# Performance work log

Hardware: AMD Instinct MI355X
Metric: run time of the kernel (lower is better)

The kernel has to match this reference:

```python
import jax, jax.numpy as jnp
import numpy as np
from jax import lax

B, D_IN, LOW_DIM, NUM_CLASS, MOCO_QUEUE = 4096, 1024, 128, 32, 65536
PROTO_M, MOCO_M, EPS = 0.99, 0.999, 1e-12


def l2norm(x, axis=-1):
    n = jnp.linalg.norm(x, axis=axis, keepdims=True)
    return x / jnp.maximum(n, EPS)


def encoder(x, W_cls, b_cls, W_proj):
    # base_encoder returns (class logits, l2-normalized low-dim embedding)
    return x @ W_cls + b_cls, l2norm(x @ W_proj)


def setup_inputs() -> dict:
    key = jax.random.key(0)
    k = jax.random.split(key, 12)
    img_q = jax.random.normal(k[0], (B, D_IN), jnp.float32)
    im_k = jax.random.normal(k[1], (B, D_IN), jnp.float32)
    true_lab = jax.random.randint(k[2], (B,), 0, NUM_CLASS)
    partial_Y = (jax.random.uniform(k[3], (B, NUM_CLASS)) < 0.3).astype(jnp.float32)
    partial_Y = partial_Y.at[jnp.arange(B), true_lab].set(1.0)  # guarantee nonempty candidate set
    W_cls_q = 0.02 * jax.random.normal(k[4], (D_IN, NUM_CLASS), jnp.float32)
    b_cls_q = jnp.zeros((NUM_CLASS,), jnp.float32)
    W_proj_q = 0.02 * jax.random.normal(k[5], (D_IN, LOW_DIM), jnp.float32)
    # key encoder initialized near query encoder (copied then momentum-drifted)
    W_cls_k = W_cls_q + 0.002 * jax.random.normal(k[6], (D_IN, NUM_CLASS), jnp.float32)
    b_cls_k = jnp.zeros((NUM_CLASS,), jnp.float32)
    W_proj_k = W_proj_q + 0.002 * jax.random.normal(k[7], (D_IN, LOW_DIM), jnp.float32)
    queue = jax.random.normal(k[8], (MOCO_QUEUE, LOW_DIM), jnp.float32)
    queue = queue / jnp.maximum(jnp.linalg.norm(queue, axis=0, keepdims=True), EPS)  # F.normalize(queue, dim=0) as in __init__
    queue_pseudo = jax.random.normal(k[9], (MOCO_QUEUE, NUM_CLASS), jnp.float32)
    queue_partial = jax.random.normal(k[10], (MOCO_QUEUE, NUM_CLASS), jnp.float32)
    prototypes = l2norm(jax.random.normal(k[11], (NUM_CLASS, LOW_DIM), jnp.float32))
    return dict(img_q=img_q, im_k=im_k, partial_Y=partial_Y,
                W_cls_q=W_cls_q, b_cls_q=b_cls_q, W_proj_q=W_proj_q,
                W_cls_k=W_cls_k, b_cls_k=b_cls_k, W_proj_k=W_proj_k,
                prototypes=prototypes, queue=queue,
                queue_pseudo=queue_pseudo, queue_partial=queue_partial)


def reference(img_q, im_k, partial_Y, W_cls_q, b_cls_q, W_proj_q,
              W_cls_k, b_cls_k, W_proj_k, prototypes, queue,
              queue_pseudo, queue_partial):
    output, q = encoder(img_q, W_cls_q, b_cls_q, W_proj_q)
    predicted_scores = jax.nn.softmax(output, axis=1) * partial_Y
    pseudo_labels = jnp.argmax(predicted_scores, axis=1)  # (B,) int
    # prototypes are detached before the similarity (clone().detach())
    score_prot = jax.nn.softmax(q @ lax.stop_gradient(prototypes).T, axis=1)
    # order-dependent per-sample EMA scatter (faithful to the python for-loop,
    # including within-batch label collisions) -> lax.scan recurrence
    qd = lax.stop_gradient(q)
    def step(p, xs):
        feat, lab = xs
        return p.at[lab].set(p[lab] * PROTO_M + (1.0 - PROTO_M) * feat), None
    new_protos, _ = lax.scan(step, lax.stop_gradient(prototypes), (qd, pseudo_labels))
    new_protos = l2norm(new_protos)
    # momentum key-encoder update (no grad), then key features
    Wck = lax.stop_gradient(W_cls_k * MOCO_M + W_cls_q * (1.0 - MOCO_M))
    bck = lax.stop_gradient(b_cls_k * MOCO_M + b_cls_q * (1.0 - MOCO_M))
    Wpk = lax.stop_gradient(W_proj_k * MOCO_M + W_proj_q * (1.0 - MOCO_M))
    _, kfeat = encoder(im_k, Wck, bck, Wpk)
    kfeat = lax.stop_gradient(kfeat)
    qv = lax.stop_gradient(queue)
    qp = lax.stop_gradient(queue_pseudo)
    qpt = lax.stop_gradient(queue_partial)
    features = jnp.concatenate([q, kfeat, qv], axis=0)
    pseudo_scores = jnp.concatenate([predicted_scores, predicted_scores, qp], axis=0)
    partial_target = jnp.concatenate([partial_Y, partial_Y, qpt], axis=0)
    # dequeue-and-enqueue at ptr=0 (buffer state update, no grad)
    new_queue = qv.at[0:B].set(kfeat)
    new_queue_pseudo = qp.at[0:B].set(lax.stop_gradient(predicted_scores))
    new_queue_partial = qpt.at[0:B].set(lax.stop_gradient(partial_Y))
    return (output, features, pseudo_scores, partial_target, score_prot,
            new_protos, new_queue, new_queue_pseudo, new_queue_partial)
```

## Files before the change

kernel.cpp:

```cpp
#include <hip/hip_runtime.h>
#include <hip/hip_bf16.h>
#include <stdint.h>


typedef __attribute__((ext_vector_type(8))) short bf16x8;
typedef __attribute__((ext_vector_type(4))) float f32x4;

constexpr size_t O0 = 0;
constexpr size_t O1 = 131072;
constexpr size_t O2 = 9568256;
constexpr size_t O3 = 11927552;
constexpr size_t O4 = 14286848;
constexpr size_t O5 = 14417920;
constexpr size_t O6 = 14422016;
constexpr size_t O7 = 22810624;
constexpr size_t O8 = 24907776;

__device__ __forceinline__ unsigned short f2b(float x) {
  union { float f; uint32_t u; } v; v.f = x;
  uint32_t u = v.u;
  uint32_t r = (u + 0x7fffu + ((u >> 16) & 1u)) >> 16;
  return (unsigned short)r;
}

__global__ __launch_bounds__(256) void prep_w(const float* __restrict__ W1,
                                              const float* __restrict__ W2,
                                              float a1, float a2, int N,
                                              unsigned short* __restrict__ Wt) {
  __shared__ float tile[32][33];
  const int kb = blockIdx.x * 32, nb = blockIdx.y * 32;
  const int tx = threadIdx.x, ty = threadIdx.y;
#pragma unroll
  for (int j = 0; j < 4; ++j) {
    const int k = kb + ty + 8 * j;
    float v = W1[(size_t)k * N + nb + tx] * a1;
    if (W2) v += W2[(size_t)k * N + nb + tx] * a2;
    tile[ty + 8 * j][tx] = v;
  }
  __syncthreads();
#pragma unroll
  for (int j = 0; j < 4; ++j) {
    const int n = nb + ty + 8 * j;
    Wt[(size_t)n * 1024 + kb + tx] = f2b(tile[tx][ty + 8 * j]);
  }
}

template <int NWAVES>
__global__ __launch_bounds__(NWAVES * 64) void gemm_enc(
    const float* __restrict__ A, const unsigned short* __restrict__ Wt,
    float* __restrict__ C) {
  constexpr int BN = NWAVES * 32;
  constexpr int NT = NWAVES * 64;
  constexpr int K = 1024;
  __shared__ __align__(16) unsigned char sA[16 * 128];
  __shared__ __align__(16) unsigned char sB[BN * 128];
  const int t = threadIdx.x;
  const int w = t >> 6, l = t & 63;
  const int ar = l & 15, kg = l >> 4;
  const int cs = w * 32;
  const int m0 = blockIdx.x * 16;
  f32x4 acc0 = {0.f, 0.f, 0.f, 0.f}, acc1 = {0.f, 0.f, 0.f, 0.f};
  for (int k0 = 0; k0 < K; k0 += 64) {
    if (t < 256) {
      const int r = t >> 4;
      const int c8 = (t & 15) * 8;
      const float4 v = *(const float4*)(A + (size_t)(m0 + r) * K + k0 + (t & 15) * 4);
      uint2 pk;
      pk.x = (uint32_t)f2b(v.x) | ((uint32_t)f2b(v.y) << 16);
      pk.y = (uint32_t)f2b(v.z) | ((uint32_t)f2b(v.w) << 16);
      *(uint2*)(sA + ((r * 128 + c8) ^ ((r & 7) << 4))) = pk;
    }
#pragma unroll
    for (int i = 0; i < (BN * 8) / NT; ++i) {
      const int cid = t + i * NT;
      const int r = cid >> 3, c = cid & 7;
      const uint4 v = *(const uint4*)(Wt + (size_t)r * K + k0 + c * 8);
      *(uint4*)(sB + ((r * 128 + c * 16) ^ ((r & 7) << 4))) = v;
    }
    __syncthreads();
#pragma unroll
    for (int s = 0; s < 2; ++s) {
      const int ch = (s * 4 + kg) * 16;
      bf16x8 a = *(const bf16x8*)(sA + ((ar * 128 + ch) ^ ((ar & 7) << 4)));
      const int r0 = cs + ar, r1 = cs + 16 + ar;
      bf16x8 b0 = *(const bf16x8*)(sB + ((r0 * 128 + ch) ^ ((r0 & 7) << 4)));
      bf16x8 b1 = *(const bf16x8*)(sB + ((r1 * 128 + ch) ^ ((r1 & 7) << 4)));
      acc0 = __builtin_amdgcn_mfma_f32_16x16x32_bf16(a, b0, acc0, 0, 0, 0);
      acc1 = __builtin_amdgcn_mfma_f32_16x16x32_bf16(a, b1, acc1, 0, 0, 0);
    }
    __syncthreads();
  }
#pragma unroll
  for (int j = 0; j < 4; ++j) {
    const int row = m0 + kg * 4 + j;
    C[(size_t)row * BN + cs + ar] = acc0[j];
    C[(size_t)row * BN + cs + 16 + ar] = acc1[j];
  }
}

__global__ __launch_bounds__(256) void post_q(
    const float* __restrict__ CQ, const float* __restrict__ bias,
    const float* __restrict__ partialY, const float* __restrict__ protos,
    float* __restrict__ out, int* __restrict__ labels) {
  __shared__ float pr[32 * 129];
  __shared__ float qs[4][128];
  const int t = threadIdx.x;
  for (int i = t; i < 4096; i += 256) pr[(i >> 7) * 129 + (i & 127)] = protos[i];
  __syncthreads();
  const int w = t >> 6, l = t & 63;
  const int row = blockIdx.x * 4 + w;
  const float* cq = CQ + (size_t)row * 160;

  float logit = -1e30f;
  if (l < 32) logit = cq[128 + l] + bias[l];
  float m = logit;
  for (int o = 32; o; o >>= 1) m = fmaxf(m, __shfl_xor(m, o));
  const float e = (l < 32) ? __expf(logit - m) : 0.f;
  float ssum = e;
  for (int o = 32; o; o >>= 1) ssum += __shfl_xor(ssum, o);
  const float py = (l < 32) ? partialY[(size_t)row * 32 + l] : 0.f;
  const float p = e / ssum * py;
  if (l < 32) {
    out[O0 + (size_t)row * 32 + l] = logit;
    out[O2 + (size_t)row * 32 + l] = p;
    out[O2 + (size_t)(4096 + row) * 32 + l] = p;
    out[O7 + (size_t)row * 32 + l] = p;
    out[O3 + (size_t)row * 32 + l] = py;
    out[O3 + (size_t)(4096 + row) * 32 + l] = py;
    out[O8 + (size_t)row * 32 + l] = py;
  }
  float av = (l < 32) ? p : -1.f;
  int ai = (l < 32) ? l : 1000;
  for (int o = 32; o; o >>= 1) {
    const float ov = __shfl_xor(av, o);
    const int oi = __shfl_xor(ai, o);
    if (ov > av || (ov == av && oi < ai)) { av = ov; ai = oi; }
  }
  if (l == 0) labels[row] = ai;

  float v0 = cq[l], v1 = cq[64 + l];
  float ss = v0 * v0 + v1 * v1;
  for (int o = 32; o; o >>= 1) ss += __shfl_xor(ss, o);
  const float den = fmaxf(sqrtf(ss), 1e-12f);
  v0 /= den; v1 /= den;
  out[O1 + (size_t)row * 128 + l] = v0;
  out[O1 + (size_t)row * 128 + 64 + l] = v1;
  qs[w][l] = v0;
  qs[w][64 + l] = v1;

  const int c = l & 31;
  const int dh = (l >> 5) * 64;
  float acc = 0.f;
#pragma unroll
  for (int d = 0; d < 64; ++d) acc += qs[w][dh + d] * pr[c * 129 + dh + d];
  acc += __shfl_xor(acc, 32);
  float sm = acc;
  for (int o = 16; o; o >>= 1) sm = fmaxf(sm, __shfl_xor(sm, o));
  const float ee = __expf(acc - sm);
  float s2 = ee;
  for (int o = 16; o; o >>= 1) s2 += __shfl_xor(s2, o);
  if (l < 32) out[O4 + (size_t)row * 32 + l] = ee / s2;
}

__global__ __launch_bounds__(256) void post_k(const float* __restrict__ CK,
                                              float* __restrict__ out) {
  const int t = threadIdx.x, w = t >> 6, l = t & 63;
  const int row = blockIdx.x * 4 + w;
  const float* ck = CK + (size_t)row * 128;
  float v0 = ck[l], v1 = ck[64 + l];
  float ss = v0 * v0 + v1 * v1;
  for (int o = 32; o; o >>= 1) ss += __shfl_xor(ss, o);
  const float den = fmaxf(sqrtf(ss), 1e-12f);
  v0 /= den; v1 /= den;
  out[O1 + (size_t)(4096 + row) * 128 + l] = v0;
  out[O1 + (size_t)(4096 + row) * 128 + 64 + l] = v1;
  out[O6 + (size_t)row * 128 + l] = v0;
  out[O6 + (size_t)row * 128 + 64 + l] = v1;
}

__global__ __launch_bounds__(128) void proto_up(const int* __restrict__ labels,
                                                const float* __restrict__ qfeat,
                                                const float* __restrict__ protos,
                                                float* __restrict__ out) {
  __shared__ int lab[4096];
  __shared__ int list[4096];
  __shared__ int cnt[128];
  __shared__ int ktot;
  __shared__ float red[2];
  const int c = blockIdx.x, t = threadIdx.x;
  for (int i = t; i < 4096; i += 128) lab[i] = labels[i];
  __syncthreads();
  int cn = 0;
#pragma unroll
  for (int j = 0; j < 32; ++j) {
    const int jj = (j + t) & 31;
    cn += (lab[t * 32 + jj] == c) ? 1 : 0;
  }
  cnt[t] = cn;
  __syncthreads();
  if (t == 0) {
    int s = 0;
    for (int i = 0; i < 128; ++i) { const int v = cnt[i]; cnt[i] = s; s += v; }
    ktot = s;
  }
  __syncthreads();
  int off = cnt[t];
  for (int j = 0; j < 32; ++j) {
    const int i = t * 32 + j;
    if (lab[i] == c) list[off++] = i;
  }
  __syncthreads();
  const int k = ktot;
  float* wf = (float*)lab;
  for (int j = t; j < k; j += 128)
    wf[j] = 0.01f * __powf(0.99f, (float)(k - 1 - j));
  __syncthreads();
  float acc = protos[(size_t)c * 128 + t] * __powf(0.99f, (float)k);
  for (int j = 0; j < k; ++j)
    acc += wf[j] * qfeat[(size_t)list[j] * 128 + t];
  float ss = acc * acc;
  for (int o = 32; o; o >>= 1) ss += __shfl_xor(ss, o);
  if ((t & 63) == 0) red[t >> 6] = ss;
  __syncthreads();
  const float tot = red[0] + red[1];
  out[O5 + (size_t)c * 128 + t] = acc / fmaxf(sqrtf(tot), 1e-12f);
}

__global__ __launch_bounds__(256) void copy_bufs(const float* __restrict__ queue,
                                                 const float* __restrict__ qp,
                                                 const float* __restrict__ qpt,
                                                 float* __restrict__ out) {
  constexpr long NQ4 = (long)65536 * 128 / 4;
  constexpr long NP4 = (long)65536 * 32 / 4;
  constexpr long TOT = NQ4 + 2 * NP4;
  float4* o4 = (float4*)out;
  for (long idx = (long)blockIdx.x * blockDim.x + threadIdx.x; idx < TOT;
       idx += (long)gridDim.x * blockDim.x) {
    if (idx < NQ4) {
      const float4 v = ((const float4*)queue)[idx];
      o4[O1 / 4 + (2L * 4096 * 128) / 4 + idx] = v;
      if ((idx >> 5) >= 4096) o4[O6 / 4 + idx] = v;
    } else if (idx < NQ4 + NP4) {
      const long i = idx - NQ4;
      const float4 v = ((const float4*)qp)[i];
      o4[O2 / 4 + (2L * 4096 * 32) / 4 + i] = v;
      if ((i >> 3) >= 4096) o4[O7 / 4 + i] = v;
    } else {
      const long i = idx - NQ4 - NP4;
      const float4 v = ((const float4*)qpt)[i];
      o4[O3 / 4 + (2L * 4096 * 32) / 4 + i] = v;
      if ((i >> 3) >= 4096) o4[O8 / 4 + i] = v;
    }
  }
}

extern "C" void kernel_launch(void* const* d_in, const int* in_sizes, int n_in,
                              void* d_out, int out_size, void* d_ws, size_t ws_size,
                              hipStream_t stream) {
  const float* img_q    = (const float*)d_in[0];
  const float* im_k     = (const float*)d_in[1];
  const float* partialY = (const float*)d_in[2];
  const float* W_cls_q  = (const float*)d_in[3];
  const float* b_cls_q  = (const float*)d_in[4];
  const float* W_proj_q = (const float*)d_in[5];
  const float* W_proj_k = (const float*)d_in[8];
  const float* protos   = (const float*)d_in[9];
  const float* queue    = (const float*)d_in[10];
  const float* queue_ps = (const float*)d_in[11];
  const float* queue_pt = (const float*)d_in[12];
  float* out = (float*)d_out;

  unsigned short* wtq = (unsigned short*)d_ws;
  unsigned short* wtk = wtq + 160 * 1024;
  float* CQ = (float*)(wtk + 128 * 1024);
  float* CK = CQ + (size_t)4096 * 160;
  int* labels = (int*)(CK + (size_t)4096 * 128);

  prep_w<<<dim3(32, 4), dim3(32, 8), 0, stream>>>(W_proj_q, nullptr, 1.0f, 0.0f, 128, wtq);
  prep_w<<<dim3(32, 1), dim3(32, 8), 0, stream>>>(W_cls_q, nullptr, 1.0f, 0.0f, 32, wtq + 128 * 1024);
  prep_w<<<dim3(32, 4), dim3(32, 8), 0, stream>>>(W_proj_k, W_proj_q, 0.999f, 0.001f, 128, wtk);
  gemm_enc<5><<<256, 320, 0, stream>>>(img_q, wtq, CQ);
  gemm_enc<4><<<256, 256, 0, stream>>>(im_k, wtk, CK);
  post_q<<<1024, 256, 0, stream>>>(CQ, b_cls_q, partialY, protos, out, labels);
  post_k<<<1024, 256, 0, stream>>>(CK, out);
  proto_up<<<32, 128, 0, stream>>>(labels, out + O1, protos, out);
  copy_bufs<<<2048, 256, 0, stream>>>(queue, queue_ps, queue_pt, out);
}
```

Baseline: 262.6 us.

## Fuse launches into prep/gemm/post kernels with split-K atomics and register prefetch

Folds the three weight-prep launches into one kernel that also zeroes the accumulation buffers, and merges both encoder GEMMs plus the classifier GEMM into a single launch. The GEMMs use split-K over two halves with atomic adds, and prefetch the next k-tile into registers while the current one is computed. The q/k postprocessing and the queue copy are merged into one launch. proto_up uses a wave-scan prefix sum and a four-way unrolled accumulation. This cuts launch count and raises GEMM parallelism, at the cost of extra zeroing traffic, atomic contention and nondeterministic summation order.

```diff
diff --git a/kernel.cpp b/kernel.cpp
--- a/kernel.cpp
+++ b/kernel.cpp
@@ -23,13 +23,34 @@
   return (unsigned short)r;
 }
 
-__global__ __launch_bounds__(256) void prep_w(const float* __restrict__ W1,
-                                              const float* __restrict__ W2,
-                                              float a1, float a2, int N,
-                                              unsigned short* __restrict__ Wt) {
+__global__ __launch_bounds__(256) void prep_zero(
+    const float* __restrict__ Wpq, const float* __restrict__ Wcq,
+    const float* __restrict__ Wpk,
+    unsigned short* __restrict__ wt_pq, unsigned short* __restrict__ wt_cls,
+    unsigned short* __restrict__ wt_pk, float* __restrict__ zbase) {
+  const int bid = blockIdx.x;
+  const int t = threadIdx.x;
+  if (bid >= 288) {
+    constexpr int ZN4 = 4096 * (128 + 32 + 128) / 4;
+    float4* z = (float4*)zbase;
+    const float4 zero = {0.f, 0.f, 0.f, 0.f};
+    for (int i = (bid - 288) * 256 + t; i < ZN4; i += 256 * 256) z[i] = zero;
+    return;
+  }
+  const float *W1, *W2 = nullptr;
+  float a1 = 1.f, a2 = 0.f;
+  unsigned short* dst;
+  int kb, nb, N;
+  if (bid < 128) {
+    W1 = Wpq; N = 128; kb = (bid & 31) * 32; nb = (bid >> 5) * 32; dst = wt_pq;
+  } else if (bid < 160) {
+    W1 = Wcq; N = 32; kb = (bid - 128) * 32; nb = 0; dst = wt_cls;
+  } else {
+    W1 = Wpk; W2 = Wpq; a1 = 0.999f; a2 = 0.001f; N = 128;
+    const int b = bid - 160; kb = (b & 31) * 32; nb = (b >> 5) * 32; dst = wt_pk;
+  }
   __shared__ float tile[32][33];
-  const int kb = blockIdx.x * 32, nb = blockIdx.y * 32;
-  const int tx = threadIdx.x, ty = threadIdx.y;
+  const int tx = t & 31, ty = t >> 5;
 #pragma unroll
   for (int j = 0; j < 4; ++j) {
     const int k = kb + ty + 8 * j;
@@ -41,141 +62,240 @@
 #pragma unroll
   for (int j = 0; j < 4; ++j) {
     const int n = nb + ty + 8 * j;
-    Wt[(size_t)n * 1024 + kb + tx] = f2b(tile[tx][ty + 8 * j]);
-  }
-}
-
-template <int NWAVES>
-__global__ __launch_bounds__(NWAVES * 64) void gemm_enc(
-    const float* __restrict__ A, const unsigned short* __restrict__ Wt,
-    float* __restrict__ C) {
-  constexpr int BN = NWAVES * 32;
-  constexpr int NT = NWAVES * 64;
-  constexpr int K = 1024;
-  __shared__ __align__(16) unsigned char sA[16 * 128];
-  __shared__ __align__(16) unsigned char sB[BN * 128];
+    dst[(size_t)n * 1024 + kb + tx] = f2b(tile[tx][ty + 8 * j]);
+  }
+}
+
+__global__ __launch_bounds__(256) void gemm_all(
+    const float* __restrict__ img_q, const float* __restrict__ im_k,
+    const unsigned short* __restrict__ wt_pq,
+    const unsigned short* __restrict__ wt_pk,
+    const unsigned short* __restrict__ wt_cls,
+    float* __restrict__ CQ, float* __restrict__ CK, float* __restrict__ CL) {
+  __shared__ __align__(16) unsigned char lds[18432];
+  const int bid = blockIdx.x;
   const int t = threadIdx.x;
   const int w = t >> 6, l = t & 63;
   const int ar = l & 15, kg = l >> 4;
-  const int cs = w * 32;
-  const int m0 = blockIdx.x * 16;
-  f32x4 acc0 = {0.f, 0.f, 0.f, 0.f}, acc1 = {0.f, 0.f, 0.f, 0.f};
-  for (int k0 = 0; k0 < K; k0 += 64) {
-    if (t < 256) {
-      const int r = t >> 4;
-      const int c8 = (t & 15) * 8;
-      const float4 v = *(const float4*)(A + (size_t)(m0 + r) * K + k0 + (t & 15) * 4);
-      uint2 pk;
-      pk.x = (uint32_t)f2b(v.x) | ((uint32_t)f2b(v.y) << 16);
-      pk.y = (uint32_t)f2b(v.z) | ((uint32_t)f2b(v.w) << 16);
-      *(uint2*)(sA + ((r * 128 + c8) ^ ((r & 7) << 4))) = pk;
-    }
-#pragma unroll
-    for (int i = 0; i < (BN * 8) / NT; ++i) {
-      const int cid = t + i * NT;
-      const int r = cid >> 3, c = cid & 7;
-      const uint4 v = *(const uint4*)(Wt + (size_t)r * K + k0 + c * 8);
-      *(uint4*)(sB + ((r * 128 + c * 16) ^ ((r & 7) << 4))) = v;
-    }
-    __syncthreads();
-#pragma unroll
-    for (int s = 0; s < 2; ++s) {
-      const int ch = (s * 4 + kg) * 16;
-      bf16x8 a = *(const bf16x8*)(sA + ((ar * 128 + ch) ^ ((ar & 7) << 4)));
-      const int r0 = cs + ar, r1 = cs + 16 + ar;
-      bf16x8 b0 = *(const bf16x8*)(sB + ((r0 * 128 + ch) ^ ((r0 & 7) << 4)));
-      bf16x8 b1 = *(const bf16x8*)(sB + ((r1 * 128 + ch) ^ ((r1 & 7) << 4)));
-      acc0 = __builtin_amdgcn_mfma_f32_16x16x32_bf16(a, b0, acc0, 0, 0, 0);
-      acc1 = __builtin_amdgcn_mfma_f32_16x16x32_bf16(a, b1, acc1, 0, 0, 0);
-    }
-    __syncthreads();
-  }
-#pragma unroll
-  for (int j = 0; j < 4; ++j) {
-    const int row = m0 + kg * 4 + j;
-    C[(size_t)row * BN + cs + ar] = acc0[j];
-    C[(size_t)row * BN + cs + 16 + ar] = acc1[j];
-  }
-}
-
-__global__ __launch_bounds__(256) void post_q(
-    const float* __restrict__ CQ, const float* __restrict__ bias,
+
+  if (bid < 1024) {
+    const bool isq = bid < 512;
+    const int b = bid & 511;
+    const int m0 = (b & 255) * 16;
+    const int kb = (b >> 8) * 512;
+    const float* A = isq ? img_q : im_k;
+    const unsigned short* Wt = isq ? wt_pq : wt_pk;
+    float* C = isq ? CQ : CK;
+    unsigned char* sA = lds;
+    unsigned char* sB = lds + 2048;
+    const int arow = t >> 4, acol = t & 15;
+    f32x4 acc0 = {0.f, 0.f, 0.f, 0.f}, acc1 = {0.f, 0.f, 0.f, 0.f};
+    float4 av; uint4 bv[4];
+    av = *(const float4*)(A + (size_t)(m0 + arow) * 1024 + kb + acol * 4);
+#pragma unroll
+    for (int i = 0; i < 4; ++i) {
+      const int cid = t + i * 256, r = cid >> 3, c = cid & 7;
+      bv[i] = *(const uint4*)(Wt + (size_t)r * 1024 + kb + c * 8);
+    }
+    for (int it = 0; it < 8; ++it) {
+      {
+        uint2 pk;
+        pk.x = (uint32_t)f2b(av.x) | ((uint32_t)f2b(av.y) << 16);
+        pk.y = (uint32_t)f2b(av.z) | ((uint32_t)f2b(av.w) << 16);
+        *(uint2*)(sA + ((arow * 128 + acol * 8) ^ ((arow & 7) << 4))) = pk;
+      }
+#pragma unroll
+      for (int i = 0; i < 4; ++i) {
+        const int cid = t + i * 256, r = cid >> 3, c = cid & 7;
+        *(uint4*)(sB + ((r * 128 + c * 16) ^ ((r & 7) << 4))) = bv[i];
+      }
+      if (it < 7) {
+        const int k0 = kb + (it + 1) * 64;
+        av = *(const float4*)(A + (size_t)(m0 + arow) * 1024 + k0 + acol * 4);
+#pragma unroll
+        for (int i = 0; i < 4; ++i) {
+          const int cid = t + i * 256, r = cid >> 3, c = cid & 7;
+          bv[i] = *(const uint4*)(Wt + (size_t)r * 1024 + k0 + c * 8);
+        }
+      }
+      __syncthreads();
+      const int cs = w * 32;
+#pragma unroll
+      for (int s = 0; s < 2; ++s) {
+        const int ch = (s * 4 + kg) * 16;
+        bf16x8 a = *(const bf16x8*)(sA + ((ar * 128 + ch) ^ ((ar & 7) << 4)));
+        const int r0 = cs + ar, r1 = cs + 16 + ar;
+        bf16x8 b0 = *(const bf16x8*)(sB + ((r0 * 128 + ch) ^ ((r0 & 7) << 4)));
+        bf16x8 b1 = *(const bf16x8*)(sB + ((r1 * 128 + ch) ^ ((r1 & 7) << 4)));
+        acc0 = __builtin_amdgcn_mfma_f32_16x16x32_bf16(a, b0, acc0, 0, 0, 0);
+        acc1 = __builtin_amdgcn_mfma_f32_16x16x32_bf16(a, b1, acc1, 0, 0, 0);
+      }
+      __syncthreads();
+    }
+    const int cs = w * 32;
+#pragma unroll
+    for (int j = 0; j < 4; ++j) {
+      const int row = m0 + kg * 4 + j;
+      unsafeAtomicAdd(&C[(size_t)row * 128 + cs + ar], acc0[j]);
+      unsafeAtomicAdd(&C[(size_t)row * 128 + cs + 16 + ar], acc1[j]);
+    }
+  } else {
+    const int b2 = bid - 1024;
+    const int m0 = (b2 & 63) * 64;
+    const int kb = (b2 >> 6) * 512;
+    unsigned char* sA = lds;
+    unsigned char* sB = lds + 8192;
+    f32x4 acc0 = {0.f, 0.f, 0.f, 0.f}, acc1 = {0.f, 0.f, 0.f, 0.f};
+    float4 av[4]; uint4 bv;
+#pragma unroll
+    for (int i = 0; i < 4; ++i) {
+      const int cid = t + i * 256, r = cid >> 4, c = cid & 15;
+      av[i] = *(const float4*)(img_q + (size_t)(m0 + r) * 1024 + kb + c * 4);
+    }
+    { const int r = t >> 3, c = t & 7;
+      bv = *(const uint4*)(wt_cls + (size_t)r * 1024 + kb + c * 8); }
+    for (int it = 0; it < 8; ++it) {
+#pragma unroll
+      for (int i = 0; i < 4; ++i) {
+        const int cid = t + i * 256, r = cid >> 4, c8 = (cid & 15) * 8;
+        uint2 pk;
+        pk.x = (uint32_t)f2b(av[i].x) | ((uint32_t)f2b(av[i].y) << 16);
+        pk.y = (uint32_t)f2b(av[i].z) | ((uint32_t)f2b(av[i].w) << 16);
+        *(uint2*)(sA + ((r * 128 + c8) ^ ((r & 7) << 4))) = pk;
+      }
+      { const int r = t >> 3, c = t & 7;
+        *(uint4*)(sB + ((r * 128 + c * 16) ^ ((r & 7) << 4))) = bv; }
+      if (it < 7) {
+        const int k0 = kb + (it + 1) * 64;
+#pragma unroll
+        for (int i = 0; i < 4; ++i) {
+          const int cid = t + i * 256, r = cid >> 4, c = cid & 15;
+          av[i] = *(const float4*)(img_q + (size_t)(m0 + r) * 1024 + k0 + c * 4);
+        }
+        const int r = t >> 3, c = t & 7;
+        bv = *(const uint4*)(wt_cls + (size_t)r * 1024 + k0 + c * 8);
+      }
+      __syncthreads();
+#pragma unroll
+      for (int s = 0; s < 2; ++s) {
+        const int ch = (s * 4 + kg) * 16;
+        const int ra = w * 16 + ar;
+        bf16x8 a = *(const bf16x8*)(sA + ((ra * 128 + ch) ^ ((ra & 7) << 4)));
+        bf16x8 b0 = *(const bf16x8*)(sB + ((ar * 128 + ch) ^ ((ar & 7) << 4)));
+        bf16x8 b1 = *(const bf16x8*)(sB + (((16 + ar) * 128 + ch) ^ ((ar & 7) << 4)));
+        acc0 = __builtin_amdgcn_mfma_f32_16x16x32_bf16(a, b0, acc0, 0, 0, 0);
+        acc1 = __builtin_amdgcn_mfma_f32_16x16x32_bf16(a, b1, acc1, 0, 0, 0);
+      }
+      __syncthreads();
+    }
+#pragma unroll
+    for (int j = 0; j < 4; ++j) {
+      const int row = m0 + w * 16 + kg * 4 + j;
+      unsafeAtomicAdd(&CL[(size_t)row * 32 + ar], acc0[j]);
+      unsafeAtomicAdd(&CL[(size_t)row * 32 + 16 + ar], acc1[j]);
+    }
+  }
+}
+
+__global__ __launch_bounds__(256) void post_all(
+    const float* __restrict__ CQ, const float* __restrict__ CL,
+    const float* __restrict__ CK, const float* __restrict__ bias,
     const float* __restrict__ partialY, const float* __restrict__ protos,
-    float* __restrict__ out, int* __restrict__ labels) {
+    const float* __restrict__ queue, const float* __restrict__ qp,
+    const float* __restrict__ qpt, float* __restrict__ out,
+    int* __restrict__ labels) {
   __shared__ float pr[32 * 129];
   __shared__ float qs[4][128];
+  const int bid = blockIdx.x;
   const int t = threadIdx.x;
-  for (int i = t; i < 4096; i += 256) pr[(i >> 7) * 129 + (i & 127)] = protos[i];
-  __syncthreads();
   const int w = t >> 6, l = t & 63;
-  const int row = blockIdx.x * 4 + w;
-  const float* cq = CQ + (size_t)row * 160;
-
-  float logit = -1e30f;
-  if (l < 32) logit = cq[128 + l] + bias[l];
-  float m = logit;
-  for (int o = 32; o; o >>= 1) m = fmaxf(m, __shfl_xor(m, o));
-  const float e = (l < 32) ? __expf(logit - m) : 0.f;
-  float ssum = e;
-  for (int o = 32; o; o >>= 1) ssum += __shfl_xor(ssum, o);
-  const float py = (l < 32) ? partialY[(size_t)row * 32 + l] : 0.f;
-  const float p = e / ssum * py;
-  if (l < 32) {
-    out[O0 + (size_t)row * 32 + l] = logit;
-    out[O2 + (size_t)row * 32 + l] = p;
-    out[O2 + (size_t)(4096 + row) * 32 + l] = p;
-    out[O7 + (size_t)row * 32 + l] = p;
-    out[O3 + (size_t)row * 32 + l] = py;
-    out[O3 + (size_t)(4096 + row) * 32 + l] = py;
-    out[O8 + (size_t)row * 32 + l] = py;
-  }
-  float av = (l < 32) ? p : -1.f;
-  int ai = (l < 32) ? l : 1000;
-  for (int o = 32; o; o >>= 1) {
-    const float ov = __shfl_xor(av, o);
-    const int oi = __shfl_xor(ai, o);
-    if (ov > av || (ov == av && oi < ai)) { av = ov; ai = oi; }
-  }
-  if (l == 0) labels[row] = ai;
-
-  float v0 = cq[l], v1 = cq[64 + l];
-  float ss = v0 * v0 + v1 * v1;
-  for (int o = 32; o; o >>= 1) ss += __shfl_xor(ss, o);
-  const float den = fmaxf(sqrtf(ss), 1e-12f);
-  v0 /= den; v1 /= den;
-  out[O1 + (size_t)row * 128 + l] = v0;
-  out[O1 + (size_t)row * 128 + 64 + l] = v1;
-  qs[w][l] = v0;
-  qs[w][64 + l] = v1;
-
-  const int c = l & 31;
-  const int dh = (l >> 5) * 64;
-  float acc = 0.f;
-#pragma unroll
-  for (int d = 0; d < 64; ++d) acc += qs[w][dh + d] * pr[c * 129 + dh + d];
-  acc += __shfl_xor(acc, 32);
-  float sm = acc;
-  for (int o = 16; o; o >>= 1) sm = fmaxf(sm, __shfl_xor(sm, o));
-  const float ee = __expf(acc - sm);
-  float s2 = ee;
-  for (int o = 16; o; o >>= 1) s2 += __shfl_xor(s2, o);
-  if (l < 32) out[O4 + (size_t)row * 32 + l] = ee / s2;
-}
-
-__global__ __launch_bounds__(256) void post_k(const float* __restrict__ CK,
-                                              float* __restrict__ out) {
-  const int t = threadIdx.x, w = t >> 6, l = t & 63;
-  const int row = blockIdx.x * 4 + w;
-  const float* ck = CK + (size_t)row * 128;
-  float v0 = ck[l], v1 = ck[64 + l];
-  float ss = v0 * v0 + v1 * v1;
-  for (int o = 32; o; o >>= 1) ss += __shfl_xor(ss, o);
-  const float den = fmaxf(sqrtf(ss), 1e-12f);
-  v0 /= den; v1 /= den;
-  out[O1 + (size_t)(4096 + row) * 128 + l] = v0;
-  out[O1 + (size_t)(4096 + row) * 128 + 64 + l] = v1;
-  out[O6 + (size_t)row * 128 + l] = v0;
-  out[O6 + (size_t)row * 128 + 64 + l] = v1;
+
+  if (bid < 1024) {
+    for (int i = t; i < 4096; i += 256) pr[(i >> 7) * 129 + (i & 127)] = protos[i];
+    __syncthreads();
+    const int row = bid * 4 + w;
+    float logit = -1e30f;
+    if (l < 32) logit = CL[(size_t)row * 32 + l] + bias[l];
+    float m = logit;
+    for (int o = 32; o; o >>= 1) m = fmaxf(m, __shfl_xor(m, o));
+    const float e = (l < 32) ? __expf(logit - m) : 0.f;
+    float ssum = e;
+    for (int o = 32; o; o >>= 1) ssum += __shfl_xor(ssum, o);
+    const float py = (l < 32) ? partialY[(size_t)row * 32 + l] : 0.f;
+    const float p = e / ssum * py;
+    if (l < 32) {
+      out[O0 + (size_t)row * 32 + l] = logit;
+      out[O2 + (size_t)row * 32 + l] = p;
+      out[O2 + (size_t)(4096 + row) * 32 + l] = p;
+      out[O7 + (size_t)row * 32 + l] = p;
+      out[O3 + (size_t)row * 32 + l] = py;
+      out[O3 + (size_t)(4096 + row) * 32 + l] = py;
+      out[O8 + (size_t)row * 32 + l] = py;
+    }
+    float av = (l < 32) ? p : -1.f;
+    int ai = (l < 32) ? l : 1000;
+    for (int o = 32; o; o >>= 1) {
+      const float ov = __shfl_xor(av, o);
+      const int oi = __shfl_xor(ai, o);
+      if (ov > av || (ov == av && oi < ai)) { av = ov; ai = oi; }
+    }
+    if (l == 0) labels[row] = ai;
+    float v0 = CQ[(size_t)row * 128 + l], v1 = CQ[(size_t)row * 128 + 64 + l];
+    float ss = v0 * v0 + v1 * v1;
+    for (int o = 32; o; o >>= 1) ss += __shfl_xor(ss, o);
+    const float den = fmaxf(sqrtf(ss), 1e-12f);
+    v0 /= den; v1 /= den;
+    out[O1 + (size_t)row * 128 + l] = v0;
+    out[O1 + (size_t)row * 128 + 64 + l] = v1;
+    qs[w][l] = v0;
+    qs[w][64 + l] = v1;
+    const int c = l & 31;
+    const int dh = (l >> 5) * 64;
+    float acc = 0.f;
+#pragma unroll
+    for (int d = 0; d < 64; ++d) acc += qs[w][dh + d] * pr[c * 129 + dh + d];
+    acc += __shfl_xor(acc, 32);
+    float sm = acc;
+    for (int o = 16; o; o >>= 1) sm = fmaxf(sm, __shfl_xor(sm, o));
+    const float ee = __expf(acc - sm);
+    float s2 = ee;
+    for (int o = 16; o; o >>= 1) s2 += __shfl_xor(s2, o);
+    if (l < 32) out[O4 + (size_t)row * 32 + l] = ee / s2;
+  } else if (bid < 2048) {
+    const int row = (bid - 1024) * 4 + w;
+    const float* ck = CK + (size_t)row * 128;
+    float v0 = ck[l], v1 = ck[64 + l];
+    float ss = v0 * v0 + v1 * v1;
+    for (int o = 32; o; o >>= 1) ss += __shfl_xor(ss, o);
+    const float den = fmaxf(sqrtf(ss), 1e-12f);
+    v0 /= den; v1 /= den;
+    out[O1 + (size_t)(4096 + row) * 128 + l] = v0;
+    out[O1 + (size_t)(4096 + row) * 128 + 64 + l] = v1;
+    out[O6 + (size_t)row * 128 + l] = v0;
+    out[O6 + (size_t)row * 128 + 64 + l] = v1;
+  } else {
+    constexpr long NQ4 = (long)65536 * 128 / 4;
+    constexpr long NP4 = (long)65536 * 32 / 4;
+    constexpr long TOT = NQ4 + 2 * NP4;
+    float4* o4 = (float4*)out;
+    for (long idx = (long)(bid - 2048) * 256 + t; idx < TOT; idx += 3072L * 256) {
+      if (idx < NQ4) {
+        const float4 v = ((const float4*)queue)[idx];
+        o4[O1 / 4 + (2L * 4096 * 128) / 4 + idx] = v;
+        if ((idx >> 5) >= 4096) o4[O6 / 4 + idx] = v;
+      } else if (idx < NQ4 + NP4) {
+        const long i = idx - NQ4;
+        const float4 v = ((const float4*)qp)[i];
+        o4[O2 / 4 + (2L * 4096 * 32) / 4 + i] = v;
+        if ((i >> 3) >= 4096) o4[O7 / 4 + i] = v;
+      } else {
+        const long i = idx - NQ4 - NP4;
+        const float4 v = ((const float4*)qpt)[i];
+        o4[O3 / 4 + (2L * 4096 * 32) / 4 + i] = v;
+        if ((i >> 3) >= 4096) o4[O8 / 4 + i] = v;
+      }
+    }
+  }
 }
 
 __global__ __launch_bounds__(128) void proto_up(const int* __restrict__ labels,
@@ -185,7 +305,6 @@
   __shared__ int lab[4096];
   __shared__ int list[4096];
   __shared__ int cnt[128];
-  __shared__ int ktot;
   __shared__ float red[2];
   const int c = blockIdx.x, t = threadIdx.x;
   for (int i = t; i < 4096; i += 128) lab[i] = labels[i];
@@ -196,62 +315,43 @@
     const int jj = (j + t) & 31;
     cn += (lab[t * 32 + jj] == c) ? 1 : 0;
   }
-  cnt[t] = cn;
-  __syncthreads();
-  if (t == 0) {
-    int s = 0;
-    for (int i = 0; i < 128; ++i) { const int v = cnt[i]; cnt[i] = s; s += v; }
-    ktot = s;
-  }
-  __syncthreads();
-  int off = cnt[t];
+  int inc = cn;
+  const int l = t & 63;
+  for (int o = 1; o < 64; o <<= 1) {
+    const int n = __shfl_up(inc, o);
+    if (l >= o) inc += n;
+  }
+  cnt[t] = inc;
+  __syncthreads();
+  const int w0tot = cnt[63];
+  const int k = cnt[127] + w0tot;
+  int off = inc - cn + ((t >= 64) ? w0tot : 0);
   for (int j = 0; j < 32; ++j) {
     const int i = t * 32 + j;
     if (lab[i] == c) list[off++] = i;
   }
   __syncthreads();
-  const int k = ktot;
   float* wf = (float*)lab;
   for (int j = t; j < k; j += 128)
     wf[j] = 0.01f * __powf(0.99f, (float)(k - 1 - j));
   __syncthreads();
-  float acc = protos[(size_t)c * 128 + t] * __powf(0.99f, (float)k);
-  for (int j = 0; j < k; ++j)
-    acc += wf[j] * qfeat[(size_t)list[j] * 128 + t];
+  float a0 = protos[(size_t)c * 128 + t] * __powf(0.99f, (float)k);
+  float a1 = 0.f, a2 = 0.f, a3 = 0.f;
+  int j = 0;
+  for (; j + 4 <= k; j += 4) {
+    a0 += wf[j]     * qfeat[(size_t)list[j] * 128 + t];
+    a1 += wf[j + 1] * qfeat[(size_t)list[j + 1] * 128 + t];
+    a2 += wf[j + 2] * qfeat[(size_t)list[j + 2] * 128 + t];
+    a3 += wf[j + 3] * qfeat[(size_t)list[j + 3] * 128 + t];
+  }
+  for (; j < k; ++j) a0 += wf[j] * qfeat[(size_t)list[j] * 128 + t];
+  const float acc = (a0 + a1) + (a2 + a3);
   float ss = acc * acc;
   for (int o = 32; o; o >>= 1) ss += __shfl_xor(ss, o);
   if ((t & 63) == 0) red[t >> 6] = ss;
   __syncthreads();
   const float tot = red[0] + red[1];
   out[O5 + (size_t)c * 128 + t] = acc / fmaxf(sqrtf(tot), 1e-12f);
-}
-
-__global__ __launch_bounds__(256) void copy_bufs(const float* __restrict__ queue,
-                                                 const float* __restrict__ qp,
-                                                 const float* __restrict__ qpt,
-                                                 float* __restrict__ out) {
-  constexpr long NQ4 = (long)65536 * 128 / 4;
-  constexpr long NP4 = (long)65536 * 32 / 4;
-  constexpr long TOT = NQ4 + 2 * NP4;
-  float4* o4 = (float4*)out;
-  for (long idx = (long)blockIdx.x * blockDim.x + threadIdx.x; idx < TOT;
-       idx += (long)gridDim.x * blockDim.x) {
-    if (idx < NQ4) {
-      const float4 v = ((const float4*)queue)[idx];
-      o4[O1 / 4 + (2L * 4096 * 128) / 4 + idx] = v;
-      if ((idx >> 5) >= 4096) o4[O6 / 4 + idx] = v;
-    } else if (idx < NQ4 + NP4) {
-      const long i = idx - NQ4;
-      const float4 v = ((const float4*)qp)[i];
-      o4[O2 / 4 + (2L * 4096 * 32) / 4 + i] = v;
-      if ((i >> 3) >= 4096) o4[O7 / 4 + i] = v;
-    } else {
-      const long i = idx - NQ4 - NP4;
-      const float4 v = ((const float4*)qpt)[i];
-      o4[O3 / 4 + (2L * 4096 * 32) / 4 + i] = v;
-      if ((i >> 3) >= 4096) o4[O8 / 4 + i] = v;
-    }
-  }
 }
 
 extern "C" void kernel_launch(void* const* d_in, const int* in_sizes, int n_in,
@@ -270,19 +370,19 @@
   const float* queue_pt = (const float*)d_in[12];
   float* out = (float*)d_out;
 
-  unsigned short* wtq = (unsigned short*)d_ws;
-  unsigned short* wtk = wtq + 160 * 1024;
-  float* CQ = (float*)(wtk + 128 * 1024);
-  float* CK = CQ + (size_t)4096 * 160;
+  unsigned short* wt_pq  = (unsigned short*)d_ws;
+  unsigned short* wt_cls = wt_pq + 128 * 1024;
+  unsigned short* wt_pk  = wt_cls + 32 * 1024;
+  float* CQ = (float*)(wt_pk + 128 * 1024);
+  float* CL = CQ + (size_t)4096 * 128;
+  float* CK = CL + (size_t)4096 * 32;
   int* labels = (int*)(CK + (size_t)4096 * 128);
 
-  prep_w<<<dim3(32, 4), dim3(32, 8), 0, stream>>>(W_proj_q, nullptr, 1.0f, 0.0f, 128, wtq);
-  prep_w<<<dim3(32, 1), dim3(32, 8), 0, stream>>>(W_cls_q, nullptr, 1.0f, 0.0f, 32, wtq + 128 * 1024);
-  prep_w<<<dim3(32, 4), dim3(32, 8), 0, stream>>>(W_proj_k, W_proj_q, 0.999f, 0.001f, 128, wtk);
-  gemm_enc<5><<<256, 320, 0, stream>>>(img_q, wtq, CQ);
-  gemm_enc<4><<<256, 256, 0, stream>>>(im_k, wtk, CK);
-  post_q<<<1024, 256, 0, stream>>>(CQ, b_cls_q, partialY, protos, out, labels);
-  post_k<<<1024, 256, 0, stream>>>(CK, out);
+  prep_zero<<<544, 256, 0, stream>>>(W_proj_q, W_cls_q, W_proj_k,
+                                     wt_pq, wt_cls, wt_pk, CQ);
+  gemm_all<<<1152, 256, 0, stream>>>(img_q, im_k, wt_pq, wt_pk, wt_cls,
+                                     CQ, CK, CL);
+  post_all<<<5120, 256, 0, stream>>>(CQ, CL, CK, b_cls_q, partialY, protos,
+                                     queue, queue_ps, queue_pt, out, labels);
   proto_up<<<32, 128, 0, stream>>>(labels, out + O1, protos, out);
-  copy_bufs<<<2048, 256, 0, stream>>>(queue, queue_ps, queue_pt, out);
-}
+}
```

Measured after the change: 251.9 us. 1.04x faster.
